# Kernel tuning notes

Hardware: AMD Instinct MI355X
Metric: run time of the kernel (lower is better)

## Reference

```python
import jax, jax.numpy as jnp
import numpy as np

B, S, H, N = 2, 2048, 1024, 16
HN = H // N  # head dim = 64
EPS = 1e-12


def setup_inputs() -> dict:
    key = jax.random.key(0)
    ks = jax.random.split(key, 8)
    scale = 0.02
    return {
        "hidden_states": jax.random.normal(ks[0], (B, S, H), dtype=jnp.float32),
        "attention_mask": jnp.zeros((B, 1, 1, S), dtype=jnp.float32),
        "W_qkv": jax.random.normal(ks[1], (3 * H, H), dtype=jnp.float32) * scale,
        "b_qkv": jnp.zeros((3 * H,), dtype=jnp.float32),
        "W_out": jax.random.normal(ks[2], (H, H), dtype=jnp.float32) * scale,
        "b_out": jnp.zeros((H,), dtype=jnp.float32),
        "ln_gamma": jnp.ones((H,), dtype=jnp.float32),
        "ln_beta": jnp.zeros((H,), dtype=jnp.float32),
    }


def reference(hidden_states, attention_mask, W_qkv, b_qkv, W_out, b_out, ln_gamma, ln_beta):
    # QKV projection: torch Linear => x @ W.T + b
    qkv = jnp.einsum("bsh,oh->bso", hidden_states, W_qkv) + b_qkv  # [B,S,3H]
    q, k, v = jnp.split(qkv, 3, axis=-1)

    def heads(t):  # [B,S,H] -> [B,N,S,HN]
        return t.reshape(B, S, N, HN).transpose(0, 2, 1, 3)

    q, k, v = heads(q), heads(k), heads(v)
    nf = jnp.sqrt(jnp.sqrt(jnp.float32(HN)))
    scores = jnp.einsum("bnsd,bntd->bnst", q / nf, k / nf) + attention_mask  # [B,N,S,S]
    probs = jax.nn.softmax(scores, axis=-1)
    ctx = jnp.einsum("bnst,bntd->bnsd", probs, v)  # [B,N,S,HN]
    ctx = ctx.transpose(0, 2, 1, 3).reshape(B, S, H)

    # output dense + residual + LayerNorm
    out = jnp.einsum("bsh,oh->bso", ctx, W_out) + b_out
    x = out + hidden_states
    mean = jnp.mean(x, axis=-1, keepdims=True)
    var = jnp.mean(jnp.square(x - mean), axis=-1, keepdims=True)
    return (x - mean) * jax.lax.rsqrt(var + EPS) * ln_gamma + ln_beta
```

## Files before the change

### kernel.cpp

```cpp
#include <hip/hip_runtime.h>
#include <hip/hip_bf16.h>
#include <math.h>

#define Bq  2
#define Sq  2048
#define Hq  1024
#define Nq  16
#define HNq 64
#define Mq  (Bq*Sq)
#define H3q (3*Hq)

#define LOG2E 1.44269504088896340736f

typedef __attribute__((ext_vector_type(8))) short           short8;
typedef __attribute__((ext_vector_type(4))) short           short4s;
typedef __attribute__((ext_vector_type(8))) unsigned short  ushortx8;
typedef __attribute__((ext_vector_type(4))) unsigned short  ushortx4;
typedef __attribute__((ext_vector_type(4))) float           floatx4;

__device__ __forceinline__ unsigned short f2bf(float f) {
    union { float f; unsigned int u; } x; x.f = f;
    unsigned int r = (x.u + 0x7fffu + ((x.u >> 16) & 1u)) >> 16;
    return (unsigned short)r;
}

__device__ __forceinline__ unsigned int pkbf(float a, float b) {
    float2 t; t.x = a; t.y = b;
    __hip_bfloat162 h = __float22bfloat162_rn(t);
    union { __hip_bfloat162 h; unsigned int u; } c; c.h = h;
    return c.u;
}

__device__ __forceinline__ float bf2f(unsigned short v) {
    union { unsigned int u; float f; } x; x.u = (unsigned int)v << 16;
    return x.f;
}

__device__ __forceinline__ void gload16(const unsigned short* g, unsigned short* l) {
    __builtin_amdgcn_global_load_lds(
        (__attribute__((address_space(1))) void*)(unsigned long long)(g),
        (__attribute__((address_space(3))) void*)(unsigned int)(unsigned long long)(l),
        16, 0, 0);
}

__device__ __forceinline__ int swz(int r) { return (r ^ (r >> 2)) & 3; }

#define N_HID ((size_t)Mq * Hq)
#define N_HW  (N_HID + (size_t)H3q * Hq)
#define N_ALL (N_HW + (size_t)Hq * Hq)

__global__ __launch_bounds__(256) void cvt_all(
    const float* __restrict__ hidden, const float* __restrict__ wqkv,
    const float* __restrict__ wout, unsigned short* __restrict__ dst)
{
    size_t i = ((size_t)blockIdx.x * 256 + threadIdx.x) * 8;
    const float* src;
    if (i < N_HID)      src = hidden + i;
    else if (i < N_HW)  src = wqkv + (i - N_HID);
    else                src = wout + (i - N_HW);
    float4 a = *(const float4*)(src);
    float4 b = *(const float4*)(src + 4);
    union { unsigned int u[4]; ushortx8 s; } o;
    o.u[0] = pkbf(a.x, a.y); o.u[1] = pkbf(a.z, a.w);
    o.u[2] = pkbf(b.x, b.y); o.u[3] = pkbf(b.z, b.w);
    *(ushortx8*)(dst + i) = o.s;
}

__global__ __launch_bounds__(256) void cvt_mask(
    const float* __restrict__ mask, unsigned short* __restrict__ em)
{
    int i = (blockIdx.x * 256 + threadIdx.x) * 8;
    union { unsigned int u[4]; ushortx8 s; } o;
    #pragma unroll
    for (int h = 0; h < 4; h++) {
        float a = exp2f(mask[i + 2*h]     * LOG2E);
        float b = exp2f(mask[i + 2*h + 1] * LOG2E);
        o.u[h] = pkbf(a, b);
    }
    *(ushortx8*)(em + i) = o.s;
}

#define TM 128
#define TN 128
#define TK 32

__global__ __launch_bounds__(256) void gemm_mfma_qkv(
    const unsigned short* __restrict__ A, const unsigned short* __restrict__ Bw,
    const float* __restrict__ bias, const float* __restrict__ mask,
    unsigned short* __restrict__ qkvC, unsigned short* __restrict__ vT,
    int M, int Nd, int K)
{
    __shared__ unsigned short As[TM][TK];
    __shared__ unsigned short Bs[TN][TK];

    const int tid = threadIdx.x;
    const int w = tid >> 6, lane = tid & 63;
    const int l15 = lane & 15, quad = lane >> 4;
    const int wr = (w & 1) * 64;
    const int wc = (w >> 1) * 64;
    const int row0 = blockIdx.y * TM;
    const int col0 = blockIdx.x * TN;

    const int srow16 = lane >> 2;
    const int sgd    = lane & 3;
    const int sgsrc  = (sgd ^ swz(srow16)) * 8;

    floatx4 acc[4][4];
    #pragma unroll
    for (int i = 0; i < 4; i++)
        #pragma unroll
        for (int j = 0; j < 4; j++) acc[i][j] = (floatx4){0.f,0.f,0.f,0.f};

    const int aswz = swz(l15) * 8;

    for (int k0 = 0; k0 < K; k0 += TK) {
        __syncthreads();
        #pragma unroll
        for (int c = 0; c < 2; c++) {
            int seg = w * 2 + c;
            int r = seg * 16 + srow16;
            gload16(A  + (size_t)(row0 + r) * K + k0 + sgsrc, &As[seg * 16][0]);
            gload16(Bw + (size_t)(col0 + r) * K + k0 + sgsrc, &Bs[seg * 16][0]);
        }
        __syncthreads();

        short8 af[4], bf[4];
        #pragma unroll
        for (int i = 0; i < 4; i++)
            af[i] = *(const short8*)&As[wr + i * 16 + l15][(quad * 8) ^ aswz];
        #pragma unroll
        for (int j = 0; j < 4; j++)
            bf[j] = *(const short8*)&Bs[wc + j * 16 + l15][(quad * 8) ^ aswz];
        #pragma unroll
        for (int i = 0; i < 4; i++)
            #pragma unroll
            for (int j = 0; j < 4; j++)
                acc[i][j] = __builtin_amdgcn_mfma_f32_16x16x32_bf16(af[i], bf[j], acc[i][j], 0, 0, 0);
    }

    const bool isV = (col0 >= 2 * Hq);

    #pragma unroll
    for (int i = 0; i < 4; i++) {
        const int rb = row0 + wr + i * 16 + quad * 4;
        const int b  = rb >> 11;
        const int s  = rb & (Sq - 1);
        float expm[4];
        if (isV) {
            #pragma unroll
            for (int rr = 0; rr < 4; rr++)
                expm[rr] = exp2f(mask[(size_t)b * Sq + s + rr] * LOG2E);
        }
        #pragma unroll
        for (int j = 0; j < 4; j++) {
            const int c = col0 + wc + j * 16 + l15;
            const float bia = bias[c];
            if (!isV) {
                const float scale = (c < Hq) ? (0.125f * LOG2E) : 1.0f;
                #pragma unroll
                for (int rr = 0; rr < 4; rr++)
                    qkvC[(size_t)(rb + rr) * Nd + c] = f2bf((acc[i][j][rr] + bia) * scale);
            } else {
                const int c2 = c - 2 * Hq;
                ushortx4 o;
                #pragma unroll
                for (int rr = 0; rr < 4; rr++)
                    o[rr] = f2bf((acc[i][j][rr] + bia) * expm[rr]);
                *(ushortx4*)&vT[((size_t)(b << 10) + c2) * Sq + s] = o;
            }
        }
    }
}

__global__ __launch_bounds__(256) void gemm_mfma_out(
    const unsigned short* __restrict__ A, const unsigned short* __restrict__ Bw,
    const float* __restrict__ bias, const float* __restrict__ res,
    unsigned short* __restrict__ X, int M, int Nd, int K)
{
    __shared__ unsigned short As[TM][TK];
    __shared__ unsigned short Bs[TN][TK];

    const int tid = threadIdx.x;
    const int w = tid >> 6, lane = tid & 63;
    const int l15 = lane & 15, quad = lane >> 4;
    const int wr = (w & 1) * 64;
    const int wc = (w >> 1) * 64;
    const int row0 = blockIdx.y * TM;
    const int col0 = blockIdx.x * TN;

    const int srow16 = lane >> 2;
    const int sgd    = lane & 3;
    const int sgsrc  = (sgd ^ swz(srow16)) * 8;

    floatx4 acc[4][4];
    #pragma unroll
    for (int i = 0; i < 4; i++)
        #pragma unroll
        for (int j = 0; j < 4; j++) acc[i][j] = (floatx4){0.f,0.f,0.f,0.f};

    const int aswz = swz(l15) * 8;

    for (int k0 = 0; k0 < K; k0 += TK) {
        __syncthreads();
        #pragma unroll
        for (int c = 0; c < 2; c++) {
            int seg = w * 2 + c;
            int r = seg * 16 + srow16;
            gload16(A  + (size_t)(row0 + r) * K + k0 + sgsrc, &As[seg * 16][0]);
            gload16(Bw + (size_t)(col0 + r) * K + k0 + sgsrc, &Bs[seg * 16][0]);
        }
        __syncthreads();

        short8 af[4], bf[4];
        #pragma unroll
        for (int i = 0; i < 4; i++)
            af[i] = *(const short8*)&As[wr + i * 16 + l15][(quad * 8) ^ aswz];
        #pragma unroll
        for (int j = 0; j < 4; j++)
            bf[j] = *(const short8*)&Bs[wc + j * 16 + l15][(quad * 8) ^ aswz];
        #pragma unroll
        for (int i = 0; i < 4; i++)
            #pragma unroll
            for (int j = 0; j < 4; j++)
                acc[i][j] = __builtin_amdgcn_mfma_f32_16x16x32_bf16(af[i], bf[j], acc[i][j], 0, 0, 0);
    }

    #pragma unroll
    for (int i = 0; i < 4; i++) {
        const int rb = row0 + wr + i * 16 + quad * 4;
        #pragma unroll
        for (int j = 0; j < 4; j++) {
            const int c = col0 + wc + j * 16 + l15;
            const float bia = bias[c];
            #pragma unroll
            for (int rr = 0; rr < 4; rr++) {
                X[(size_t)(rb + rr) * Nd + c] =
                    f2bf(acc[i][j][rr] + bia + res[(size_t)(rb + rr) * Nd + c]);
            }
        }
    }
}

#define KTILES 16

__global__ __launch_bounds__(256) void attn_mfma(
    const unsigned short* __restrict__ qkv, const unsigned short* __restrict__ vT,
    const unsigned short* __restrict__ expmask, unsigned short* __restrict__ Opart,
    float* __restrict__ Lpart)
{
    __shared__ unsigned short Ks[64][64];
    __shared__ unsigned short Vt[64][64];
    __shared__ unsigned short maskE[64];

    const int tid  = threadIdx.x;
    const int w    = tid >> 6;
    const int lane = tid & 63;
    const int l15  = lane & 15;
    const int quad = lane >> 4;

    const int qtile = blockIdx.x;
    const int bn    = blockIdx.y;
    const int z     = blockIdx.z;
    const int n     = bn & 15;
    const int b     = bn >> 4;

    const int qoff = n * HNq;
    const int koff = Hq + n * HNq;
    const int kbase = z * (KTILES * 64);

    short8 qfrag0[2], qfrag1[2];
    {
        const int qrow0 = qtile * 128 + w * 16 + l15;
        const unsigned short* qp = qkv + (size_t)(b * Sq + qrow0) * H3q + qoff + quad * 8;
        qfrag0[0] = *(const short8*)(qp);
        qfrag0[1] = *(const short8*)(qp + 32);
        qp += (size_t)64 * H3q;
        qfrag1[0] = *(const short8*)(qp);
        qfrag1[1] = *(const short8*)(qp + 32);
    }

    floatx4 oacc0[4], oacc1[4];
    #pragma unroll
    for (int dt = 0; dt < 4; dt++) {
        oacc0[dt] = (floatx4){0.f,0.f,0.f,0.f};
        oacc1[dt] = (floatx4){0.f,0.f,0.f,0.f};
    }
    floatx4 lacc0 = (floatx4){0.f,0.f,0.f,0.f};
    floatx4 lacc1 = (floatx4){0.f,0.f,0.f,0.f};

    const int krow8 = lane >> 3;
    const int kgr   = (lane & 7) ^ (krow8 & 7);
    const unsigned short* kp0 = qkv + (size_t)(b * Sq + kbase + w * 16 + krow8) * H3q + koff + kgr * 8;
    const unsigned short* kp1 = kp0 + (size_t)8 * H3q;
    unsigned short* kd0 = &Ks[w * 16][0];
    unsigned short* kd1 = &Ks[w * 16 + 8][0];
    const size_t kstep = (size_t)64 * H3q;

    const int vd0 = tid >> 3,        vg0 = tid & 7;
    const int vd1 = 32 + (tid >> 3), vg1 = tid & 7;
    const unsigned short* vbase = vT + (size_t)(b * Nq + n) * HNq * Sq;
    const unsigned short* ebase = expmask + (size_t)b * Sq;

    ushortx8 vreg0, vreg1;
    ushortx4 ereg;
    {
        vreg0 = *(const ushortx8*)(vbase + (size_t)vd0 * Sq + kbase + vg0 * 8);
        vreg1 = *(const ushortx8*)(vbase + (size_t)vd1 * Sq + kbase + vg1 * 8);
        if (tid < 16) ereg = *(const ushortx4*)(ebase + kbase + tid * 4);
    }

    for (int kt = 0; kt < KTILES; kt++) {
        __syncthreads();
        gload16(kp0, kd0);
        gload16(kp1, kd1);
        kp0 += kstep; kp1 += kstep;
        *(ushortx8*)&Vt[vd0][(vg0 ^ (vd0 & 7)) * 8] = vreg0;
        *(ushortx8*)&Vt[vd1][(vg1 ^ (vd1 & 7)) * 8] = vreg1;
        if (tid < 16) *(ushortx4*)&maskE[tid * 4] = ereg;
        __syncthreads();

        if (kt + 1 < KTILES) {
            const int nk0 = kbase + (kt + 1) * 64;
            vreg0 = *(const ushortx8*)(vbase + (size_t)vd0 * Sq + nk0 + vg0 * 8);
            vreg1 = *(const ushortx8*)(vbase + (size_t)vd1 * Sq + nk0 + vg1 * 8);
            if (tid < 16) ereg = *(const ushortx4*)(ebase + nk0 + tid * 4);
        }

        floatx4 sacc0[4], sacc1[4];
        #pragma unroll
        for (int ct = 0; ct < 4; ct++) {
            sacc0[ct] = (floatx4){0.f,0.f,0.f,0.f};
            sacc1[ct] = (floatx4){0.f,0.f,0.f,0.f};
        }
        #pragma unroll
        for (int ks = 0; ks < 2; ks++) {
            #pragma unroll
            for (int ct = 0; ct < 4; ct++) {
                short8 af = *(const short8*)&Ks[ct * 16 + l15][((4 * ks + quad) ^ (l15 & 7)) * 8];
                sacc0[ct] = __builtin_amdgcn_mfma_f32_16x16x32_bf16(af, qfrag0[ks], sacc0[ct], 0, 0, 0);
                sacc1[ct] = __builtin_amdgcn_mfma_f32_16x16x32_bf16(af, qfrag1[ks], sacc1[ct], 0, 0, 0);
            }
        }

        short8 pf0[2], pf1[2];
        #pragma unroll
        for (int ks = 0; ks < 2; ks++) {
            union { unsigned int u[4]; short8 s; } pk;
            #pragma unroll
            for (int h = 0; h < 2; h++) {
                const int ct = ks * 2 + h;
                pk.u[h * 2]     = pkbf(exp2f(sacc0[ct][0]), exp2f(sacc0[ct][1]));
                pk.u[h * 2 + 1] = pkbf(exp2f(sacc0[ct][2]), exp2f(sacc0[ct][3]));
            }
            pf0[ks] = pk.s;
        }
        #pragma unroll
        for (int ks = 0; ks < 2; ks++) {
            union { unsigned int u[4]; short8 s; } pk;
            #pragma unroll
            for (int h = 0; h < 2; h++) {
                const int ct = ks * 2 + h;
                pk.u[h * 2]     = pkbf(exp2f(sacc1[ct][0]), exp2f(sacc1[ct][1]));
                pk.u[h * 2 + 1] = pkbf(exp2f(sacc1[ct][2]), exp2f(sacc1[ct][3]));
            }
            pf1[ks] = pk.s;
        }

        #pragma unroll
        for (int ks = 0; ks < 2; ks++) {
            short4s mlo = *(const short4s*)&maskE[32 * ks + quad * 4];
            short4s mhi = *(const short4s*)&maskE[32 * ks + 16 + quad * 4];
            short8 mf = __builtin_shufflevector(mlo, mhi, 0, 1, 2, 3, 4, 5, 6, 7);
            lacc0 = __builtin_amdgcn_mfma_f32_16x16x32_bf16(mf, pf0[ks], lacc0, 0, 0, 0);
            lacc1 = __builtin_amdgcn_mfma_f32_16x16x32_bf16(mf, pf1[ks], lacc1, 0, 0, 0);
        }

        #pragma unroll
        for (int ks = 0; ks < 2; ks++) {
            const int c0 = (((4 * ks +     (quad >> 1)) ^ (l15 & 7)) * 8) + (quad & 1) * 4;
            const int c1 = (((4 * ks + 2 + (quad >> 1)) ^ (l15 & 7)) * 8) + (quad & 1) * 4;
            #pragma unroll
            for (int dt = 0; dt < 4; dt++) {
                const int d = dt * 16 + l15;
                short4s lo = *(const short4s*)&Vt[d][c0];
                short4s hi = *(const short4s*)&Vt[d][c1];
                short8 vf = __builtin_shufflevector(lo, hi, 0, 1, 2, 3, 4, 5, 6, 7);
                oacc0[dt] = __builtin_amdgcn_mfma_f32_16x16x32_bf16(vf, pf0[ks], oacc0[dt], 0, 0, 0);
                oacc1[dt] = __builtin_amdgcn_mfma_f32_16x16x32_bf16(vf, pf1[ks], oacc1[dt], 0, 0, 0);
            }
        }
    }

    unsigned short* Ow = Opart + (size_t)z * Mq * Hq;
    #pragma unroll
    for (int sub = 0; sub < 2; sub++) {
        const float l_i = sub ? lacc1[0] : lacc0[0];
        const int qrow = qtile * 128 + sub * 64 + w * 16 + l15;
        if (quad == 0)
            Lpart[(size_t)z * Mq * Nq + (size_t)(b * Sq + qrow) * Nq + n] = l_i;
        #pragma unroll
        for (int dt = 0; dt < 4; dt++) {
            const floatx4 oa = sub ? oacc1[dt] : oacc0[dt];
            union { unsigned int u[2]; ushortx4 s; } o;
            o.u[0] = pkbf(oa[0], oa[1]);
            o.u[1] = pkbf(oa[2], oa[3]);
            const int col = n * HNq + dt * 16 + quad * 4;
            *(ushortx4*)&Ow[(size_t)(b * Sq + qrow) * Hq + col] = o.s;
        }
    }
}

__global__ __launch_bounds__(256) void attn_merge(
    const unsigned short* __restrict__ Opart, const float* __restrict__ Lpart,
    unsigned short* __restrict__ ctx)
{
    const size_t idx = ((size_t)blockIdx.x * 256 + threadIdx.x) * 4;
    const int row = (int)(idx >> 10);
    const int n   = ((int)idx >> 6) & 15;
    const float l = Lpart[(size_t)row * Nq + n]
                  + Lpart[(size_t)Mq * Nq + (size_t)row * Nq + n];
    const float inv = 1.0f / l;
    ushortx4 a = *(const ushortx4*)(Opart + idx);
    ushortx4 c = *(const ushortx4*)(Opart + (size_t)Mq * Hq + idx);
    union { unsigned int u[2]; ushortx4 s; } o;
    o.u[0] = pkbf((bf2f(a[0]) + bf2f(c[0])) * inv, (bf2f(a[1]) + bf2f(c[1])) * inv);
    o.u[1] = pkbf((bf2f(a[2]) + bf2f(c[2])) * inv, (bf2f(a[3]) + bf2f(c[3])) * inv);
    *(ushortx4*)(ctx + idx) = o.s;
}

__global__ __launch_bounds__(256) void ln_kernel(
    const unsigned short* __restrict__ X, const float* __restrict__ gamma,
    const float* __restrict__ beta, float* __restrict__ out)
{
    const int row = blockIdx.x;
    const int c0  = threadIdx.x * 4;
    ushortx4 xv = *(const ushortx4*)(X + (size_t)row * Hq + c0);
    float vals[4];
    float lsum = 0.0f;
    #pragma unroll
    for (int i = 0; i < 4; i++) { vals[i] = bf2f(xv[i]); lsum += vals[i]; }

    __shared__ float red[8];
    const int wid = threadIdx.x >> 6, lane = threadIdx.x & 63;

    float s = lsum;
    #pragma unroll
    for (int off = 32; off >= 1; off >>= 1) s += __shfl_xor(s, off, 64);
    if (lane == 0) red[wid] = s;
    __syncthreads();
    const float mean = (red[0] + red[1] + red[2] + red[3]) * (1.0f / Hq);

    float v = 0.0f;
    #pragma unroll
    for (int i = 0; i < 4; i++) { float d = vals[i] - mean; v += d * d; }
    #pragma unroll
    for (int off = 32; off >= 1; off >>= 1) v += __shfl_xor(v, off, 64);
    if (lane == 0) red[4 + wid] = v;
    __syncthreads();
    const float var  = (red[4] + red[5] + red[6] + red[7]) * (1.0f / Hq);
    const float rstd = rsqrtf(var + 1e-12f);

    float4 gm = *(const float4*)(gamma + c0);
    float4 bt = *(const float4*)(beta + c0);
    float4 o;
    o.x = (vals[0] - mean) * rstd * gm.x + bt.x;
    o.y = (vals[1] - mean) * rstd * gm.y + bt.y;
    o.z = (vals[2] - mean) * rstd * gm.z + bt.z;
    o.w = (vals[3] - mean) * rstd * gm.w + bt.w;
    *(float4*)(out + (size_t)row * Hq + c0) = o;
}

extern "C" void kernel_launch(void* const* d_in, const int* in_sizes, int n_in,
                              void* d_out, int out_size, void* d_ws, size_t ws_size,
                              hipStream_t stream)
{
    const float* hidden = (const float*)d_in[0];
    const float* mask   = (const float*)d_in[1];
    const float* W_qkv  = (const float*)d_in[2];
    const float* b_qkv  = (const float*)d_in[3];
    const float* W_out  = (const float*)d_in[4];
    const float* b_out  = (const float*)d_in[5];
    const float* gamma  = (const float*)d_in[6];
    const float* beta   = (const float*)d_in[7];
    float* out = (float*)d_out;

    const size_t nHid  = (size_t)Mq * Hq;
    const size_t nWq   = (size_t)H3q * Hq;
    const size_t nWo   = (size_t)Hq * Hq;
    const size_t nQKV  = (size_t)Mq * H3q;
    const size_t nVT   = (size_t)Bq * Hq * Sq;
    const size_t nCtx  = (size_t)Mq * Hq;

    unsigned short* hidden_bf = (unsigned short*)d_ws;
    unsigned short* Wqkv_bf   = hidden_bf + nHid;
    unsigned short* Wout_bf   = Wqkv_bf + nWq;
    unsigned short* qkv_bf    = Wout_bf + nWo;
    unsigned short* vT        = qkv_bf + nQKV;
    unsigned short* ctx_bf    = vT + nVT;
    unsigned short* x_bf      = ctx_bf + nCtx;
    unsigned short* opart     = x_bf + nHid;
    float*          lpart     = (float*)(opart + 2 * nHid);
    unsigned short* expm_bf   = (unsigned short*)(lpart + 2 * (size_t)Mq * Nq);

    dim3 blk(256);

    cvt_all<<<dim3((int)(N_ALL / 2048)), blk, 0, stream>>>(
        hidden, W_qkv, W_out, hidden_bf);
    cvt_mask<<<dim3(2), blk, 0, stream>>>(mask, expm_bf);

    gemm_mfma_qkv<<<dim3(H3q / TN, Mq / TM), blk, 0, stream>>>(
        hidden_bf, Wqkv_bf, b_qkv, mask, qkv_bf, vT, Mq, H3q, Hq);

    attn_mfma<<<dim3(Sq / 128, Bq * Nq, 2), blk, 0, stream>>>(
        qkv_bf, vT, expm_bf, opart, lpart);

    attn_merge<<<dim3((int)(nCtx / 1024)), blk, 0, stream>>>(
        opart, lpart, ctx_bf);

    gemm_mfma_out<<<dim3(Hq / TN, Mq / TM), blk, 0, stream>>>(
        ctx_bf, Wout_bf, b_out, hidden, x_bf, Mq, Hq, Hq);

    ln_kernel<<<dim3(Mq), blk, 0, stream>>>(x_bf, gamma, beta, out);
}
```

Baseline: 237.1 us.

## Split QKV output into Q/K/V buffers with fragment-ordered V layout and double-buffered K

The QKV GEMM epilogue now writes Q and K into separate contiguous [M,H] buffers and writes V in a tiled layout that matches the MFMA operand fragments. The attention kernel then loads V fragments and mask values straight from global memory into registers, so it no longer stages V and the mask through shared memory. K is double-buffered in LDS, which leaves one barrier per iteration instead of two. The aim is to cut LDS traffic and barrier stalls in the attention loop. In exchange the V tile is read uncached through global loads each step, and the epilogue for V does scattered 8-byte stores.

```diff
diff --git a/kernel.cpp b/kernel.cpp
--- a/kernel.cpp
+++ b/kernel.cpp
@@ -87,8 +87,8 @@
 __global__ __launch_bounds__(256) void gemm_mfma_qkv(
     const unsigned short* __restrict__ A, const unsigned short* __restrict__ Bw,
     const float* __restrict__ bias, const float* __restrict__ mask,
-    unsigned short* __restrict__ qkvC, unsigned short* __restrict__ vT,
-    int M, int Nd, int K)
+    unsigned short* __restrict__ Qb, unsigned short* __restrict__ Kd,
+    unsigned short* __restrict__ V5, int K)
 {
     __shared__ unsigned short As[TM][TK];
     __shared__ unsigned short Bs[TN][TK];
@@ -138,35 +138,48 @@
                 acc[i][j] = __builtin_amdgcn_mfma_f32_16x16x32_bf16(af[i], bf[j], acc[i][j], 0, 0, 0);
     }
 
-    const bool isV = (col0 >= 2 * Hq);
-
-    #pragma unroll
-    for (int i = 0; i < 4; i++) {
-        const int rb = row0 + wr + i * 16 + quad * 4;
-        const int b  = rb >> 11;
-        const int s  = rb & (Sq - 1);
-        float expm[4];
-        if (isV) {
+    const int cls = col0 >> 10;
+
+    if (cls == 2) {
+        #pragma unroll
+        for (int i = 0; i < 4; i++) {
+            const int rb = row0 + wr + i * 16 + quad * 4;
+            const int b  = rb >> 11;
+            const int s  = rb & (Sq - 1);
+            float expm[4];
             #pragma unroll
             for (int rr = 0; rr < 4; rr++)
                 expm[rr] = exp2f(mask[(size_t)b * Sq + s + rr] * LOG2E);
-        }
-        #pragma unroll
-        for (int j = 0; j < 4; j++) {
-            const int c = col0 + wc + j * 16 + l15;
-            const float bia = bias[c];
-            if (!isV) {
-                const float scale = (c < Hq) ? (0.125f * LOG2E) : 1.0f;
-                #pragma unroll
-                for (int rr = 0; rr < 4; rr++)
-                    qkvC[(size_t)(rb + rr) * Nd + c] = f2bf((acc[i][j][rr] + bia) * scale);
-            } else {
+            #pragma unroll
+            for (int j = 0; j < 4; j++) {
+                const int c  = col0 + wc + j * 16 + l15;
                 const int c2 = c - 2 * Hq;
+                const int n  = c2 >> 6, d = c2 & 63;
+                const float bia = bias[c];
                 ushortx4 o;
                 #pragma unroll
                 for (int rr = 0; rr < 4; rr++)
                     o[rr] = f2bf((acc[i][j][rr] + bia) * expm[rr]);
-                *(ushortx4*)&vT[((size_t)(b << 10) + c2) * Sq + s] = o;
+                const size_t off = ((((size_t)(b * Nq + n)) * 32 + (s >> 6)) << 12)
+                                 + (size_t)((((s >> 2) & 15) << 8) + ((d & 15) << 4) + ((d >> 4) << 2));
+                *(ushortx4*)&V5[off] = o;
+            }
+        }
+    } else {
+        unsigned short* __restrict__ dst = (cls == 0) ? Qb : Kd;
+        const int cshift = (cls == 0) ? 0 : Hq;
+        const float qs = (cls == 0) ? (0.125f * LOG2E) : 1.0f;
+        #pragma unroll
+        for (int i = 0; i < 4; i++) {
+            const int rb = row0 + wr + i * 16 + quad * 4;
+            #pragma unroll
+            for (int j = 0; j < 4; j++) {
+                const int c = col0 + wc + j * 16 + l15;
+                const float bia = bias[c];
+                #pragma unroll
+                for (int rr = 0; rr < 4; rr++)
+                    dst[(size_t)(rb + rr) * Hq + (c - cshift)] =
+                        f2bf((acc[i][j][rr] + bia) * qs);
             }
         }
     }
@@ -244,13 +257,11 @@
 #define KTILES 16
 
 __global__ __launch_bounds__(256) void attn_mfma(
-    const unsigned short* __restrict__ qkv, const unsigned short* __restrict__ vT,
-    const unsigned short* __restrict__ expmask, unsigned short* __restrict__ Opart,
-    float* __restrict__ Lpart)
-{
-    __shared__ unsigned short Ks[64][64];
-    __shared__ unsigned short Vt[64][64];
-    __shared__ unsigned short maskE[64];
+    const unsigned short* __restrict__ Qb, const unsigned short* __restrict__ Kd,
+    const unsigned short* __restrict__ V5, const unsigned short* __restrict__ expmask,
+    unsigned short* __restrict__ Opart, float* __restrict__ Lpart)
+{
+    __shared__ unsigned short Ks[2][64][64];
 
     const int tid  = threadIdx.x;
     const int w    = tid >> 6;
@@ -264,17 +275,15 @@
     const int n     = bn & 15;
     const int b     = bn >> 4;
 
-    const int qoff = n * HNq;
-    const int koff = Hq + n * HNq;
     const int kbase = z * (KTILES * 64);
 
     short8 qfrag0[2], qfrag1[2];
     {
         const int qrow0 = qtile * 128 + w * 16 + l15;
-        const unsigned short* qp = qkv + (size_t)(b * Sq + qrow0) * H3q + qoff + quad * 8;
+        const unsigned short* qp = Qb + (size_t)(b * Sq + qrow0) * Hq + n * HNq + quad * 8;
         qfrag0[0] = *(const short8*)(qp);
         qfrag0[1] = *(const short8*)(qp + 32);
-        qp += (size_t)64 * H3q;
+        qp += (size_t)64 * Hq;
         qfrag1[0] = *(const short8*)(qp);
         qfrag1[1] = *(const short8*)(qp + 32);
     }
@@ -290,40 +299,45 @@
 
     const int krow8 = lane >> 3;
     const int kgr   = (lane & 7) ^ (krow8 & 7);
-    const unsigned short* kp0 = qkv + (size_t)(b * Sq + kbase + w * 16 + krow8) * H3q + koff + kgr * 8;
-    const unsigned short* kp1 = kp0 + (size_t)8 * H3q;
-    unsigned short* kd0 = &Ks[w * 16][0];
-    unsigned short* kd1 = &Ks[w * 16 + 8][0];
-    const size_t kstep = (size_t)64 * H3q;
-
-    const int vd0 = tid >> 3,        vg0 = tid & 7;
-    const int vd1 = 32 + (tid >> 3), vg1 = tid & 7;
-    const unsigned short* vbase = vT + (size_t)(b * Nq + n) * HNq * Sq;
-    const unsigned short* ebase = expmask + (size_t)b * Sq;
-
-    ushortx8 vreg0, vreg1;
-    ushortx4 ereg;
-    {
-        vreg0 = *(const ushortx8*)(vbase + (size_t)vd0 * Sq + kbase + vg0 * 8);
-        vreg1 = *(const ushortx8*)(vbase + (size_t)vd1 * Sq + kbase + vg1 * 8);
-        if (tid < 16) ereg = *(const ushortx4*)(ebase + kbase + tid * 4);
-    }
-
+    const unsigned short* kp = Kd + (size_t)(b * Sq + kbase + w * 16 + krow8) * Hq
+                                  + n * HNq + kgr * 8;
+    const size_t kstep = (size_t)64 * Hq;
+
+    gload16(kp,                   &Ks[0][w * 16][0]);
+    gload16(kp + (size_t)8 * Hq,  &Ks[0][w * 16 + 8][0]);
+
+    const unsigned short* Vb = V5 + ((size_t)(b * Nq + n) * 32 + z * KTILES) * 4096;
+    const unsigned short* eb = expmask + (size_t)b * Sq + kbase;
+    const int vfo = quad * 256 + l15 * 16;
+
+    #pragma unroll 2
     for (int kt = 0; kt < KTILES; kt++) {
-        __syncthreads();
-        gload16(kp0, kd0);
-        gload16(kp1, kd1);
-        kp0 += kstep; kp1 += kstep;
-        *(ushortx8*)&Vt[vd0][(vg0 ^ (vd0 & 7)) * 8] = vreg0;
-        *(ushortx8*)&Vt[vd1][(vg1 ^ (vd1 & 7)) * 8] = vreg1;
-        if (tid < 16) *(ushortx4*)&maskE[tid * 4] = ereg;
-        __syncthreads();
-
+        asm volatile("s_waitcnt vmcnt(0)" ::: "memory");
+        __builtin_amdgcn_s_barrier();
+        __builtin_amdgcn_sched_barrier(0);
+
+        const int cur = kt & 1;
         if (kt + 1 < KTILES) {
-            const int nk0 = kbase + (kt + 1) * 64;
-            vreg0 = *(const ushortx8*)(vbase + (size_t)vd0 * Sq + nk0 + vg0 * 8);
-            vreg1 = *(const ushortx8*)(vbase + (size_t)vd1 * Sq + nk0 + vg1 * 8);
-            if (tid < 16) ereg = *(const ushortx4*)(ebase + nk0 + tid * 4);
+            const unsigned short* kpn = kp + (size_t)(kt + 1) * kstep;
+            gload16(kpn,                  &Ks[cur ^ 1][w * 16][0]);
+            gload16(kpn + (size_t)8 * Hq, &Ks[cur ^ 1][w * 16 + 8][0]);
+        }
+
+        const unsigned short* vt = Vb + (size_t)kt * 4096;
+        short8 vA[2], vB[2], wA[2], wB[2];
+        #pragma unroll
+        for (int ks = 0; ks < 2; ks++) {
+            const int o = ks * 2048 + vfo;
+            vA[ks] = *(const short8*)(vt + o);
+            vB[ks] = *(const short8*)(vt + o + 8);
+            wA[ks] = *(const short8*)(vt + o + 1024);
+            wB[ks] = *(const short8*)(vt + o + 1032);
+        }
+        short4s ml[2], mh[2];
+        #pragma unroll
+        for (int ks = 0; ks < 2; ks++) {
+            ml[ks] = *(const short4s*)(eb + kt * 64 + 32 * ks + quad * 4);
+            mh[ks] = *(const short4s*)(eb + kt * 64 + 32 * ks + 16 + quad * 4);
         }
 
         floatx4 sacc0[4], sacc1[4];
@@ -336,7 +350,7 @@
         for (int ks = 0; ks < 2; ks++) {
             #pragma unroll
             for (int ct = 0; ct < 4; ct++) {
-                short8 af = *(const short8*)&Ks[ct * 16 + l15][((4 * ks + quad) ^ (l15 & 7)) * 8];
+                short8 af = *(const short8*)&Ks[cur][ct * 16 + l15][((4 * ks + quad) ^ (l15 & 7)) * 8];
                 sacc0[ct] = __builtin_amdgcn_mfma_f32_16x16x32_bf16(af, qfrag0[ks], sacc0[ct], 0, 0, 0);
                 sacc1[ct] = __builtin_amdgcn_mfma_f32_16x16x32_bf16(af, qfrag1[ks], sacc1[ct], 0, 0, 0);
             }
@@ -368,26 +382,25 @@
 
         #pragma unroll
         for (int ks = 0; ks < 2; ks++) {
-            short4s mlo = *(const short4s*)&maskE[32 * ks + quad * 4];
-            short4s mhi = *(const short4s*)&maskE[32 * ks + 16 + quad * 4];
-            short8 mf = __builtin_shufflevector(mlo, mhi, 0, 1, 2, 3, 4, 5, 6, 7);
+            short8 mf = __builtin_shufflevector(ml[ks], mh[ks], 0, 1, 2, 3, 4, 5, 6, 7);
             lacc0 = __builtin_amdgcn_mfma_f32_16x16x32_bf16(mf, pf0[ks], lacc0, 0, 0, 0);
             lacc1 = __builtin_amdgcn_mfma_f32_16x16x32_bf16(mf, pf1[ks], lacc1, 0, 0, 0);
         }
 
         #pragma unroll
         for (int ks = 0; ks < 2; ks++) {
-            const int c0 = (((4 * ks +     (quad >> 1)) ^ (l15 & 7)) * 8) + (quad & 1) * 4;
-            const int c1 = (((4 * ks + 2 + (quad >> 1)) ^ (l15 & 7)) * 8) + (quad & 1) * 4;
-            #pragma unroll
-            for (int dt = 0; dt < 4; dt++) {
-                const int d = dt * 16 + l15;
-                short4s lo = *(const short4s*)&Vt[d][c0];
-                short4s hi = *(const short4s*)&Vt[d][c1];
-                short8 vf = __builtin_shufflevector(lo, hi, 0, 1, 2, 3, 4, 5, 6, 7);
-                oacc0[dt] = __builtin_amdgcn_mfma_f32_16x16x32_bf16(vf, pf0[ks], oacc0[dt], 0, 0, 0);
-                oacc1[dt] = __builtin_amdgcn_mfma_f32_16x16x32_bf16(vf, pf1[ks], oacc1[dt], 0, 0, 0);
-            }
+            short8 vf0 = __builtin_shufflevector(vA[ks], wA[ks], 0, 1, 2, 3, 8, 9, 10, 11);
+            short8 vf1 = __builtin_shufflevector(vA[ks], wA[ks], 4, 5, 6, 7, 12, 13, 14, 15);
+            short8 vf2 = __builtin_shufflevector(vB[ks], wB[ks], 0, 1, 2, 3, 8, 9, 10, 11);
+            short8 vf3 = __builtin_shufflevector(vB[ks], wB[ks], 4, 5, 6, 7, 12, 13, 14, 15);
+            oacc0[0] = __builtin_amdgcn_mfma_f32_16x16x32_bf16(vf0, pf0[ks], oacc0[0], 0, 0, 0);
+            oacc1[0] = __builtin_amdgcn_mfma_f32_16x16x32_bf16(vf0, pf1[ks], oacc1[0], 0, 0, 0);
+            oacc0[1] = __builtin_amdgcn_mfma_f32_16x16x32_bf16(vf1, pf0[ks], oacc0[1], 0, 0, 0);
+            oacc1[1] = __builtin_amdgcn_mfma_f32_16x16x32_bf16(vf1, pf1[ks], oacc1[1], 0, 0, 0);
+            oacc0[2] = __builtin_amdgcn_mfma_f32_16x16x32_bf16(vf2, pf0[ks], oacc0[2], 0, 0, 0);
+            oacc1[2] = __builtin_amdgcn_mfma_f32_16x16x32_bf16(vf2, pf1[ks], oacc1[2], 0, 0, 0);
+            oacc0[3] = __builtin_amdgcn_mfma_f32_16x16x32_bf16(vf3, pf0[ks], oacc0[3], 0, 0, 0);
+            oacc1[3] = __builtin_amdgcn_mfma_f32_16x16x32_bf16(vf3, pf1[ks], oacc1[3], 0, 0, 0);
         }
     }
 
@@ -487,16 +500,15 @@
     const size_t nHid  = (size_t)Mq * Hq;
     const size_t nWq   = (size_t)H3q * Hq;
     const size_t nWo   = (size_t)Hq * Hq;
-    const size_t nQKV  = (size_t)Mq * H3q;
-    const size_t nVT   = (size_t)Bq * Hq * Sq;
     const size_t nCtx  = (size_t)Mq * Hq;
 
     unsigned short* hidden_bf = (unsigned short*)d_ws;
     unsigned short* Wqkv_bf   = hidden_bf + nHid;
     unsigned short* Wout_bf   = Wqkv_bf + nWq;
-    unsigned short* qkv_bf    = Wout_bf + nWo;
-    unsigned short* vT        = qkv_bf + nQKV;
-    unsigned short* ctx_bf    = vT + nVT;
+    unsigned short* qb        = Wout_bf + nWo;
+    unsigned short* kd        = qb + nHid;
+    unsigned short* v5        = kd + nHid;
+    unsigned short* ctx_bf    = v5 + nHid;
     unsigned short* x_bf      = ctx_bf + nCtx;
     unsigned short* opart     = x_bf + nHid;
     float*          lpart     = (float*)(opart + 2 * nHid);
@@ -509,10 +521,10 @@
     cvt_mask<<<dim3(2), blk, 0, stream>>>(mask, expm_bf);
 
     gemm_mfma_qkv<<<dim3(H3q / TN, Mq / TM), blk, 0, stream>>>(
-        hidden_bf, Wqkv_bf, b_qkv, mask, qkv_bf, vT, Mq, H3q, Hq);
+        hidden_bf, Wqkv_bf, b_qkv, mask, qb, kd, v5, Hq);
 
     attn_mfma<<<dim3(Sq / 128, Bq * Nq, 2), blk, 0, stream>>>(
-        qkv_bf, vT, expm_bf, opart, lpart);
+        qb, kd, v5, expm_bf, opart, lpart);
 
     attn_merge<<<dim3((int)(nCtx / 1024)), blk, 0, stream>>>(
         opart, lpart, ctx_bf);
```

Result: slower. 248.1 us (+4.7%).
